# Optimization experiments

Measured on AMD Instinct MI355X. Metric: run time of the kernel, lower is better.

The kernel has to match this reference:

```python
import jax, jax.numpy as jnp
import numpy as np

N = 50000      # nodes
E = 400000     # edges (before self-loops)
DIN = 128
HID = 128
HEADS = 4
DOUT = 64
NEG_SLOPE = 0.2  # PyG GATConv default


def setup_inputs() -> dict:
    key = jax.random.key(0)
    ks = jax.random.split(key, 14)

    def w(k, shape, fan_in):
        return jax.random.normal(k, shape, dtype=jnp.float32) * (1.0 / np.sqrt(fan_in))

    x = jax.random.normal(ks[0], (N, DIN), dtype=jnp.float32)
    edge_index = jax.random.randint(ks[1], (2, E), 0, N, dtype=jnp.int32)

    # layer 1: DIN -> HEADS*HID (concat)
    W1 = w(ks[2], (DIN, HEADS * HID), DIN)
    a_src1 = w(ks[3], (HEADS, HID), HID)
    a_dst1 = w(ks[4], (HEADS, HID), HID)
    b1 = jnp.zeros((HEADS * HID,), jnp.float32)
    # layer 2: HEADS*HID -> HEADS*HID (concat)
    W2 = w(ks[5], (HEADS * HID, HEADS * HID), HEADS * HID)
    a_src2 = w(ks[6], (HEADS, HID), HID)
    a_dst2 = w(ks[7], (HEADS, HID), HID)
    b2 = jnp.zeros((HEADS * HID,), jnp.float32)
    # layer 3: HEADS*HID -> DOUT, heads=1, concat=False (mean)
    W3 = w(ks[8], (HEADS * HID, DOUT), HEADS * HID)
    a_src3 = w(ks[9], (1, DOUT), DOUT)
    a_dst3 = w(ks[10], (1, DOUT), DOUT)
    b3 = jnp.zeros((DOUT,), jnp.float32)

    return dict(x=x, edge_index=edge_index,
                W1=W1, a_src1=a_src1, a_dst1=a_dst1, b1=b1,
                W2=W2, a_src2=a_src2, a_dst2=a_dst2, b2=b2,
                W3=W3, a_src3=a_src3, a_dst3=a_dst3, b3=b3)


def _gat_layer(x, src, dst, W, a_src, a_dst, n):
    """One GATConv (eval mode, self-loops already in src/dst). Returns [n, H, C]."""
    H, C = a_src.shape
    h = (x @ W).reshape(n, H, C)                        # projected features
    alpha_s = jnp.einsum('nhc,hc->nh', h, a_src)        # per-node src logits
    alpha_d = jnp.einsum('nhc,hc->nh', h, a_dst)
    e = jax.nn.leaky_relu(alpha_s[src] + alpha_d[dst], NEG_SLOPE)  # [E', H]
    # segment softmax over incoming edges of each dst node
    m = jax.ops.segment_max(e, dst, num_segments=n)
    e = jnp.exp(e - m[dst])
    s = jax.ops.segment_sum(e, dst, num_segments=n)
    alpha = e / (s[dst] + 1e-16)                        # [E', H]
    msg = h[src] * alpha[:, :, None]                    # [E', H, C]
    return jax.ops.segment_sum(msg, dst, num_segments=n)


def reference(x, edge_index, W1, a_src1, a_dst1, b1,
              W2, a_src2, a_dst2, b2, W3, a_src3, a_dst3, b3):
    n = x.shape[0]
    loops = jnp.arange(n, dtype=edge_index.dtype)       # PyG add_self_loops=True
    src = jnp.concatenate([edge_index[0], loops])
    dst = jnp.concatenate([edge_index[1], loops])

    h = _gat_layer(x, src, dst, W1, a_src1, a_dst1, n).reshape(n, -1) + b1
    h = jax.nn.elu(h)   # dropout is identity in eval mode
    h = _gat_layer(h, src, dst, W2, a_src2, a_dst2, n).reshape(n, -1) + b2
    h = jax.nn.elu(h)
    out = _gat_layer(h, src, dst, W3, a_src3, a_dst3, n)[:, 0, :] + b3  # heads=1, concat=False
    return out
```

## Files before the change

kernel.cpp:

```cpp
#include <hip/hip_runtime.h>
#include <hip/hip_bf16.h>


typedef __attribute__((ext_vector_type(8))) short bf16x8;
typedef __attribute__((ext_vector_type(4))) float f32x4;

__device__ __forceinline__ float bflo(unsigned w) { return __uint_as_float(w << 16); }
__device__ __forceinline__ float bfhi(unsigned w) { return __uint_as_float(w & 0xffff0000u); }
__device__ __forceinline__ float leaky(float x) { return x > 0.f ? x : 0.2f * x; }
__device__ __forceinline__ unsigned pack2(float a, float b) {
    unsigned ua = __bfloat16_as_ushort(__float2bfloat16(a));
    unsigned ub = __bfloat16_as_ushort(__float2bfloat16(b));
    return ua | (ub << 16);
}


__global__ void k_count(const int* __restrict__ ei, int E, int N, int* __restrict__ cnt) {
    int e = blockIdx.x * blockDim.x + threadIdx.x;
    int tot = E + N;
    if (e >= tot) return;
    int d = (e < E) ? ei[E + e] : (e - E);
    atomicAdd(&cnt[d], 1);
}

__global__ void k_scan1(const int* __restrict__ cnt, int N, int* __restrict__ rp,
                        int* __restrict__ blksum) {
    __shared__ int sdata[256];
    int t = threadIdx.x;
    int base = blockIdx.x * 1024;
    int v[4];
    int loc = 0;
#pragma unroll
    for (int i = 0; i < 4; i++) {
        int idx = base + t * 4 + i;
        v[i] = (idx < N) ? ((cnt[idx] + 3) & ~3) : 0;
        loc += v[i];
    }
    int x = loc;
    sdata[t] = x;
    __syncthreads();
    for (int off = 1; off < 256; off <<= 1) {
        int y = (t >= off) ? sdata[t - off] : 0;
        __syncthreads();
        x += y;
        sdata[t] = x;
        __syncthreads();
    }
    int run = x - loc;
#pragma unroll
    for (int i = 0; i < 4; i++) {
        int idx = base + t * 4 + i;
        if (idx < N) rp[idx] = run;
        run += v[i];
    }
    if (t == 255) blksum[blockIdx.x] = x;
}

__global__ void k_scan2(const int* __restrict__ blksum, int nblk, int* __restrict__ blkoff) {
    int l = threadIdx.x;
    int v = (l < nblk) ? blksum[l] : 0;
    int x = v;
#pragma unroll
    for (int off = 1; off < 64; off <<= 1) {
        int y = __shfl_up(x, off);
        if (l >= off) x += y;
    }
    if (l < nblk) blkoff[l] = x - v;
}

__global__ void k_scan3(int* __restrict__ rp, const int* __restrict__ blkoff,
                        const int* __restrict__ blksum, const int* __restrict__ cnt,
                        int N, int nblk, int* __restrict__ cur,
                        int* __restrict__ col, int* __restrict__ dste) {
    int i = blockIdx.x * blockDim.x + threadIdx.x;
    if (i < N) {
        int v = rp[i] + blkoff[i >> 10];
        rp[i] = v;
        cur[i] = v;
        int c = cnt[i];
        int pad = ((c + 3) & ~3) - c;
        for (int p = 0; p < pad; p++) {
            col[v + c + p] = 0;
            dste[v + c + p] = -1;
        }
    }
    if (i == 0) rp[N] = blkoff[nblk - 1] + blksum[nblk - 1];
}

__global__ void k_fill(const int* __restrict__ ei, int E, int N, int* __restrict__ cur,
                       int* __restrict__ col, int* __restrict__ dste) {
    int e = blockIdx.x * blockDim.x + threadIdx.x;
    int tot = E + N;
    if (e >= tot) return;
    int s, d;
    if (e < E) { s = ei[e]; d = ei[E + e]; }
    else       { s = e - E; d = e - E; }
    int p = atomicAdd(&cur[d], 1);
    col[p] = s;
    dste[p] = d;
}


__global__ void k_cast_pad(const float* __restrict__ X, __hip_bfloat16* __restrict__ Xb,
                           int n_elems, int total) {
    int i = (blockIdx.x * blockDim.x + threadIdx.x) * 4;
    if (i >= total) return;
    float4 v = make_float4(0.f, 0.f, 0.f, 0.f);
    if (i < n_elems) v = *(const float4*)&X[i];
    __hip_bfloat16 tmp[4] = {__float2bfloat16(v.x), __float2bfloat16(v.y),
                             __float2bfloat16(v.z), __float2bfloat16(v.w)};
    *(ushort4*)&Xb[i] = *(const ushort4*)tmp;
}

__global__ void k_castT(const float* __restrict__ W, __hip_bfloat16* __restrict__ Wt,
                        int K, int Nw) {
    __shared__ float t[32][33];
    int k0 = blockIdx.x * 32, n0 = blockIdx.y * 32;
    int tx = threadIdx.x & 31, ty = threadIdx.x >> 5;
    for (int i = ty; i < 32; i += 8) t[i][tx] = W[(size_t)(k0 + i) * Nw + n0 + tx];
    __syncthreads();
    for (int i = ty; i < 32; i += 8)
        Wt[(size_t)(n0 + i) * K + k0 + tx] = __float2bfloat16(t[tx][i]);
}

__global__ void k_va1(const float* __restrict__ W1, const float* __restrict__ asrc,
                      const float* __restrict__ adst, float* __restrict__ va8) {
    int t = threadIdx.x;
    int c = t >> 2, h = t & 3;
    const float* wrow = W1 + (size_t)c * 512 + h * 128;
    const float* av = asrc + h * 128;
    const float* dv = adst + h * 128;
    float vs = 0.f, vd = 0.f;
    for (int k = 0; k < 128; k++) {
        float wv = wrow[k];
        vs += wv * av[k];
        vd += wv * dv[k];
    }
    va8[c * 8 + h] = vs;
    va8[c * 8 + 4 + h] = vd;
}

__global__ void k_alpha_x(const __hip_bfloat16* __restrict__ xb,
                          const float* __restrict__ va8, float* __restrict__ as_out,
                          float* __restrict__ ad_out, int N) {
    int w = (blockIdx.x * blockDim.x + threadIdx.x) >> 6;
    int lane = threadIdx.x & 63;
    if (w >= N) return;
    unsigned wrd = ((const unsigned*)xb)[(size_t)w * 64 + lane];
    float f0 = bflo(wrd), f1 = bfhi(wrd);
    int c0 = lane * 2;
    float4 vs0 = *(const float4*)&va8[c0 * 8];
    float4 vd0 = *(const float4*)&va8[c0 * 8 + 4];
    float4 vs1 = *(const float4*)&va8[(c0 + 1) * 8];
    float4 vd1 = *(const float4*)&va8[(c0 + 1) * 8 + 4];
    float s[8];
    s[0] = f0 * vs0.x + f1 * vs1.x;
    s[1] = f0 * vs0.y + f1 * vs1.y;
    s[2] = f0 * vs0.z + f1 * vs1.z;
    s[3] = f0 * vs0.w + f1 * vs1.w;
    s[4] = f0 * vd0.x + f1 * vd1.x;
    s[5] = f0 * vd0.y + f1 * vd1.y;
    s[6] = f0 * vd0.z + f1 * vd1.z;
    s[7] = f0 * vd0.w + f1 * vd1.w;
#pragma unroll
    for (int off = 32; off >= 1; off >>= 1)
#pragma unroll
        for (int j = 0; j < 8; j++) s[j] += __shfl_xor(s[j], off);
    if (lane == 0) {
        *(float4*)&as_out[w * 4] = make_float4(s[0], s[1], s[2], s[3]);
        *(float4*)&ad_out[w * 4] = make_float4(s[4], s[5], s[6], s[7]);
    }
}


template <int BN, bool FUSE>
__global__ void __launch_bounds__(256) k_gemm_mfma(const __hip_bfloat16* __restrict__ A,
                                                   const __hip_bfloat16* __restrict__ Bt,
                                                   __hip_bfloat16* __restrict__ C,
                                                   int lda, int ldc, int K,
                                                   int hsA, int hsB, int hsC,
                                                   const float* __restrict__ bias) {
    constexpr int BM = 128, BK = 64;
    constexpr int WM = 64;
    constexpr int WN = BN / 2;
    constexpr int MREP = WM / 16;
    constexpr int NREP = WN / 16;

    __shared__ __hip_bfloat16 lds[(BM + BN) * BK];
    __hip_bfloat16* As = lds;
    __hip_bfloat16* Bs = lds + BM * BK;

    const int z = blockIdx.z;
    A += (size_t)z * hsA;
    Bt += (size_t)z * hsB;
    const int cbase = z * hsC;

    const int tid = threadIdx.x;
    const int wave = tid >> 6;
    const int lane = tid & 63;
    const int wm0 = (wave >> 1) * WM;
    const int wn0 = (wave & 1) * WN;
    const int m0 = blockIdx.y * BM;
    const int n0 = blockIdx.x * BN;
    const int fr = lane & 15;
    const int fq = lane >> 4;

    f32x4 acc[MREP][NREP] = {};

    for (int kt = 0; kt < K; kt += BK) {
        const __hip_bfloat16* srcA = A + (size_t)m0 * lda + kt;
#pragma unroll
        for (int it = 0; it < BM * 8 / 256; ++it) {
            int gb = it * 256 + wave * 64;
            int g = gb + lane;
            int row = g >> 3;
            int kg = (g & 7) ^ (row & 7);
            const __hip_bfloat16* gsrc = srcA + (size_t)row * lda + kg * 8;
            __builtin_amdgcn_global_load_lds(
                (const __attribute__((address_space(1))) void*)gsrc,
                (__attribute__((address_space(3))) void*)(As + gb * 8), 16, 0, 0);
        }
        const __hip_bfloat16* srcB = Bt + (size_t)n0 * K + kt;
#pragma unroll
        for (int it = 0; it < BN * 8 / 256; ++it) {
            int gb = it * 256 + wave * 64;
            int g = gb + lane;
            int row = g >> 3;
            int kg = (g & 7) ^ (row & 7);
            const __hip_bfloat16* gsrc = srcB + (size_t)row * K + kg * 8;
            __builtin_amdgcn_global_load_lds(
                (const __attribute__((address_space(1))) void*)gsrc,
                (__attribute__((address_space(3))) void*)(Bs + gb * 8), 16, 0, 0);
        }
        __syncthreads();

#pragma unroll
        for (int sl = 0; sl < 2; ++sl) {
            int ke = sl * 32 + fq * 8;
            bf16x8 af[MREP], bfr[NREP];
#pragma unroll
            for (int i = 0; i < MREP; ++i) {
                int row = wm0 + i * 16 + fr;
                int e = (row * BK + ke) ^ ((row & 7) << 3);
                af[i] = *(const bf16x8*)(As + e);
            }
#pragma unroll
            for (int j = 0; j < NREP; ++j) {
                int row = wn0 + j * 16 + fr;
                int e = (row * BK + ke) ^ ((row & 7) << 3);
                bfr[j] = *(const bf16x8*)(Bs + e);
            }
#pragma unroll
            for (int i = 0; i < MREP; ++i)
#pragma unroll
                for (int j = 0; j < NREP; ++j)
                    acc[i][j] = __builtin_amdgcn_mfma_f32_16x16x32_bf16(
                        af[i], bfr[j], acc[i][j], 0, 0, 0);
        }
        __syncthreads();
    }

#pragma unroll
    for (int i = 0; i < MREP; ++i) {
#pragma unroll
        for (int j = 0; j < NREP; ++j) {
            int colg = cbase + n0 + wn0 + j * 16 + fr;
#pragma unroll
            for (int r = 0; r < 4; ++r) {
                int rowg = m0 + wm0 + i * 16 + fq * 4 + r;
                float v = acc[i][j][r];
                if (FUSE) {
                    v += bias[colg];
                    v = v > 0.f ? v : expm1f(v);
                }
                C[(size_t)rowg * ldc + colg] = __float2bfloat16(v);
            }
        }
    }
}


template <int C, int H>
__global__ void k_alpha(const __hip_bfloat16* __restrict__ h, const float* __restrict__ a_src,
                        const float* __restrict__ a_dst, float* __restrict__ as_out,
                        float* __restrict__ ad_out, int N) {
    int w = (blockIdx.x * blockDim.x + threadIdx.x) >> 6;
    int lane = threadIdx.x & 63;
    int n = w / H, hd = w % H;
    if (n >= N) return;
    const __hip_bfloat16* hp = h + (size_t)n * (C * H) + hd * C;
    const float* asp = a_src + hd * C;
    const float* adp = a_dst + hd * C;
    float s1 = 0.f, s2 = 0.f;
    if constexpr (C == 128) {
        unsigned wrd = *(const unsigned*)(hp + 2 * lane);
        float f0 = bflo(wrd), f1 = bfhi(wrd);
        float2 a2 = *(const float2*)(asp + 2 * lane);
        float2 d2 = *(const float2*)(adp + 2 * lane);
        s1 = f0 * a2.x + f1 * a2.y;
        s2 = f0 * d2.x + f1 * d2.y;
    } else {
        float v = __bfloat162float(hp[lane & 63]);
        s1 = v * asp[lane];
        s2 = v * adp[lane];
    }
#pragma unroll
    for (int off = 32; off >= 1; off >>= 1) {
        s1 += __shfl_xor(s1, off);
        s2 += __shfl_xor(s2, off);
    }
    if (lane == 0) {
        as_out[n * H + hd] = s1;
        ad_out[n * H + hd] = s2;
    }
}


__global__ void k_edgewA(const int* __restrict__ col, const int* __restrict__ dste,
                         const float* __restrict__ as, const float* __restrict__ ad,
                         float* __restrict__ wA, const int* __restrict__ rp, int N) {
    int e = blockIdx.x * blockDim.x + threadIdx.x;
    if (e >= rp[N]) return;
    int d = dste[e];
    if (d < 0) {
        *(float4*)&wA[e * 4] = make_float4(0.f, 0.f, 0.f, 0.f);
        return;
    }
    int s = col[e];
    float4 a = *(const float4*)&as[s * 4];
    float4 b = *(const float4*)&ad[d * 4];
    float4 w;
    w.x = __expf(leaky(a.x + b.x));
    w.y = __expf(leaky(a.y + b.y));
    w.z = __expf(leaky(a.z + b.z));
    w.w = __expf(leaky(a.w + b.w));
    *(float4*)&wA[e * 4] = w;
}


__global__ void k_edgewS(const int* __restrict__ col, const int* __restrict__ dste,
                         const float* __restrict__ as, const float* __restrict__ ad,
                         float* __restrict__ wS, const int* __restrict__ rp, int N, int EP) {
    int e = blockIdx.x * blockDim.x + threadIdx.x;
    if (e >= rp[N]) return;
    int d = dste[e];
    if (d < 0) {
        wS[e] = 0.f; wS[EP + e] = 0.f; wS[2 * EP + e] = 0.f; wS[3 * EP + e] = 0.f;
        return;
    }
    int s = col[e];
    float4 a = *(const float4*)&as[s * 4];
    float4 b = *(const float4*)&ad[d * 4];
    wS[e]          = __expf(leaky(a.x + b.x));
    wS[EP + e]     = __expf(leaky(a.y + b.y));
    wS[2 * EP + e] = __expf(leaky(a.z + b.z));
    wS[3 * EP + e] = __expf(leaky(a.w + b.w));
}

__global__ void k_edgew1(const int* __restrict__ col, const int* __restrict__ dste,
                         const float* __restrict__ as, const float* __restrict__ ad,
                         float* __restrict__ wS, const int* __restrict__ rp, int N) {
    int e = blockIdx.x * blockDim.x + threadIdx.x;
    if (e >= rp[N]) return;
    int d = dste[e];
    if (d < 0) { wS[e] = 0.f; return; }
    wS[e] = __expf(leaky(as[col[e]] + ad[d]));
}


__global__ void k_gatherX(const __hip_bfloat16* __restrict__ xb,
                          const float* __restrict__ wA, const int* __restrict__ rp,
                          const int* __restrict__ col, unsigned* __restrict__ out32, int N) {
    int w = (blockIdx.x * blockDim.x + threadIdx.x) >> 6;
    int lane = threadIdx.x & 63;
    if (w >= N) return;
    int d = w;
    int r0 = rp[d], r1 = rp[d + 1];
    const unsigned* xp = (const unsigned*)xb;

    float acc[8] = {};
    float ws0 = 0.f, ws1 = 0.f, ws2 = 0.f, ws3 = 0.f;
    for (int e = r0; e < r1; e += 4) {
        int4 c4 = *(const int4*)&col[e];
        float4 w0 = *(const float4*)&wA[e * 4];
        float4 w1 = *(const float4*)&wA[e * 4 + 4];
        float4 w2 = *(const float4*)&wA[e * 4 + 8];
        float4 w3 = *(const float4*)&wA[e * 4 + 12];
        unsigned v0 = xp[(size_t)c4.x * 64 + lane];
        unsigned v1 = xp[(size_t)c4.y * 64 + lane];
        unsigned v2 = xp[(size_t)c4.z * 64 + lane];
        unsigned v3 = xp[(size_t)c4.w * 64 + lane];
        ws0 += w0.x + w1.x + w2.x + w3.x;
        ws1 += w0.y + w1.y + w2.y + w3.y;
        ws2 += w0.z + w1.z + w2.z + w3.z;
        ws3 += w0.w + w1.w + w2.w + w3.w;
        float f0, f1;
        f0 = bflo(v0); f1 = bfhi(v0);
        acc[0] += w0.x * f0; acc[1] += w0.x * f1;
        acc[2] += w0.y * f0; acc[3] += w0.y * f1;
        acc[4] += w0.z * f0; acc[5] += w0.z * f1;
        acc[6] += w0.w * f0; acc[7] += w0.w * f1;
        f0 = bflo(v1); f1 = bfhi(v1);
        acc[0] += w1.x * f0; acc[1] += w1.x * f1;
        acc[2] += w1.y * f0; acc[3] += w1.y * f1;
        acc[4] += w1.z * f0; acc[5] += w1.z * f1;
        acc[6] += w1.w * f0; acc[7] += w1.w * f1;
        f0 = bflo(v2); f1 = bfhi(v2);
        acc[0] += w2.x * f0; acc[1] += w2.x * f1;
        acc[2] += w2.y * f0; acc[3] += w2.y * f1;
        acc[4] += w2.z * f0; acc[5] += w2.z * f1;
        acc[6] += w2.w * f0; acc[7] += w2.w * f1;
        f0 = bflo(v3); f1 = bfhi(v3);
        acc[0] += w3.x * f0; acc[1] += w3.x * f1;
        acc[2] += w3.y * f0; acc[3] += w3.y * f1;
        acc[4] += w3.z * f0; acc[5] += w3.z * f1;
        acc[6] += w3.w * f0; acc[7] += w3.w * f1;
    }
    float i0 = 1.f / (ws0 + 1e-16f), i1 = 1.f / (ws1 + 1e-16f);
    float i2 = 1.f / (ws2 + 1e-16f), i3 = 1.f / (ws3 + 1e-16f);
    size_t ob = (size_t)d * 256 + lane;
    out32[ob]       = pack2(acc[0] * i0, acc[1] * i0);
    out32[ob + 64]  = pack2(acc[2] * i1, acc[3] * i1);
    out32[ob + 128] = pack2(acc[4] * i2, acc[5] * i2);
    out32[ob + 192] = pack2(acc[6] * i3, acc[7] * i3);
}


__global__ void k_gatherH(const __hip_bfloat16* __restrict__ hfeat,
                          const float* __restrict__ wS, const int* __restrict__ rp,
                          const int* __restrict__ col, const float* __restrict__ bias,
                          unsigned* __restrict__ out32, int N, int EP) {
    int w = (blockIdx.x * blockDim.x + threadIdx.x) >> 6;
    int lane = threadIdx.x & 63;
    if (w >= N) return;
    int hd = blockIdx.z;
    int d = w;
    int r0 = rp[d], r1 = rp[d + 1];
    const float* wp = wS + (size_t)hd * EP;
    const unsigned* hp = (const unsigned*)hfeat;
    const int coff = hd * 64 + lane;

    float a0 = 0.f, a1 = 0.f, wsum = 0.f;
    for (int e = r0; e < r1; e += 4) {
        int4 c4 = *(const int4*)&col[e];
        float4 w4 = *(const float4*)&wp[e];
        unsigned v0 = hp[(size_t)c4.x * 256 + coff];
        unsigned v1 = hp[(size_t)c4.y * 256 + coff];
        unsigned v2 = hp[(size_t)c4.z * 256 + coff];
        unsigned v3 = hp[(size_t)c4.w * 256 + coff];
        wsum += (w4.x + w4.y) + (w4.z + w4.w);
        a0 += w4.x * bflo(v0); a1 += w4.x * bfhi(v0);
        a0 += w4.y * bflo(v1); a1 += w4.y * bfhi(v1);
        a0 += w4.z * bflo(v2); a1 += w4.z * bfhi(v2);
        a0 += w4.w * bflo(v3); a1 += w4.w * bfhi(v3);
    }
    float inv = 1.f / (wsum + 1e-16f);
    int c = hd * 128 + lane * 2;
    float o0 = a0 * inv + bias[c];
    float o1 = a1 * inv + bias[c + 1];
    o0 = o0 > 0.f ? o0 : expm1f(o0);
    o1 = o1 > 0.f ? o1 : expm1f(o1);
    out32[(size_t)d * 256 + coff] = pack2(o0, o1);
}


__global__ void k_gather64(const __hip_bfloat16* __restrict__ hfeat,
                           const float* __restrict__ wbuf, const int* __restrict__ rp,
                           const int* __restrict__ col, const float* __restrict__ bias,
                           float* __restrict__ out, int N) {
    int w = (blockIdx.x * blockDim.x + threadIdx.x) >> 6;
    int lane = threadIdx.x & 63;
    if (w >= N) return;
    int d = w;
    int r0 = rp[d], r1 = rp[d + 1];
    int g = lane >> 4, cl = lane & 15;

    float a0 = 0.f, a1 = 0.f, a2 = 0.f, a3 = 0.f, wsum = 0.f;
    for (int e0 = r0; e0 < r1; e0 += 4) {
        int e = e0 + g;
        int s = col[e];
        float wf = wbuf[e];
        uint2 q = *(const uint2*)(hfeat + (size_t)s * 64 + cl * 4);
        wsum += wf;
        a0 += wf * bflo(q.x);
        a1 += wf * bfhi(q.x);
        a2 += wf * bflo(q.y);
        a3 += wf * bfhi(q.y);
    }
#pragma unroll
    for (int off = 16; off <= 32; off <<= 1) {
        a0 += __shfl_xor(a0, off);
        a1 += __shfl_xor(a1, off);
        a2 += __shfl_xor(a2, off);
        a3 += __shfl_xor(a3, off);
        wsum += __shfl_xor(wsum, off);
    }
    if (g == 0) {
        float inv = 1.0f / (wsum + 1e-16f);
        float4 b4 = *(const float4*)&bias[cl * 4];
        float4 o = make_float4(a0 * inv + b4.x, a1 * inv + b4.y,
                               a2 * inv + b4.z, a3 * inv + b4.w);
        *(float4*)(out + (size_t)d * 64 + cl * 4) = o;
    }
}


extern "C" void kernel_launch(void* const* d_in, const int* in_sizes, int n_in,
                              void* d_out, int out_size, void* d_ws, size_t ws_size,
                              hipStream_t stream) {
    const float* x   = (const float*)d_in[0];
    const int*   ei  = (const int*)d_in[1];
    const float* W1  = (const float*)d_in[2];
    const float* as1 = (const float*)d_in[3];
    const float* ad1 = (const float*)d_in[4];
    const float* b1  = (const float*)d_in[5];
    const float* W2  = (const float*)d_in[6];
    const float* as2 = (const float*)d_in[7];
    const float* ad2 = (const float*)d_in[8];
    const float* b2  = (const float*)d_in[9];
    const float* W3  = (const float*)d_in[10];
    const float* as3 = (const float*)d_in[11];
    const float* ad3 = (const float*)d_in[12];
    const float* b3  = (const float*)d_in[13];

    const int N = in_sizes[0] / 128;
    const int E = in_sizes[1] / 2;
    const int Etot = E + N;
    const int EP = (Etot + 3 * N + 255) & ~255;
    const int Mp = (N + 127) & ~127;

    char* ws = (char*)d_ws;
    size_t off = 0;
    auto alloc = [&](size_t bytes) -> void* {
        void* p = ws + off;
        off = (off + bytes + 255) & ~(size_t)255;
        return p;
    };
    __hip_bfloat16* hbuf = (__hip_bfloat16*)alloc((size_t)Mp * 512 * 2);
    __hip_bfloat16* fbuf = (__hip_bfloat16*)alloc((size_t)Mp * 512 * 2);
    __hip_bfloat16* xagg = (__hip_bfloat16*)alloc((size_t)Mp * 512 * 2);
    __hip_bfloat16* xb   = (__hip_bfloat16*)alloc((size_t)Mp * 128 * 2);
    __hip_bfloat16* Wt1  = (__hip_bfloat16*)alloc((size_t)512 * 128 * 2);
    __hip_bfloat16* Wt2  = (__hip_bfloat16*)alloc((size_t)512 * 512 * 2);
    __hip_bfloat16* Wt3  = (__hip_bfloat16*)alloc((size_t)64 * 512 * 2);
    float* aS   = (float*)alloc((size_t)N * 4 * 4);
    float* aD   = (float*)alloc((size_t)N * 4 * 4);
    float* wbuf = (float*)alloc((size_t)EP * 4 * 4);
    float* va8  = (float*)alloc(128 * 8 * 4);
    int* cnt  = (int*)alloc((size_t)N * 4);
    int* rp   = (int*)alloc((size_t)(N + 1) * 4);
    int* cur  = (int*)alloc((size_t)N * 4);
    int* col  = (int*)alloc((size_t)EP * 4);
    int* dste = (int*)alloc((size_t)EP * 4);
    int* blks = (int*)alloc(64 * 4);
    int* blko = (int*)alloc(64 * 4);

    hipMemsetAsync(cnt, 0, (size_t)N * 4, stream);
    int thr = 256;
    k_count<<<(Etot + thr - 1) / thr, thr, 0, stream>>>(ei, E, N, cnt);
    int nblk = (N + 1023) / 1024;
    k_scan1<<<nblk, 256, 0, stream>>>(cnt, N, rp, blks);
    k_scan2<<<1, 64, 0, stream>>>(blks, nblk, blko);
    k_scan3<<<(N + 255) / 256, 256, 0, stream>>>(rp, blko, blks, cnt, N, nblk, cur, col, dste);
    k_fill<<<(Etot + thr - 1) / thr, thr, 0, stream>>>(ei, E, N, cur, col, dste);

    {
        int total = Mp * 128;
        k_cast_pad<<<(total / 4 + 255) / 256, 256, 0, stream>>>(x, xb, N * 128, total);
        dim3 g1(128 / 32, 512 / 32);
        k_castT<<<g1, 256, 0, stream>>>(W1, Wt1, 128, 512);
        dim3 g2(512 / 32, 512 / 32);
        k_castT<<<g2, 256, 0, stream>>>(W2, Wt2, 512, 512);
        dim3 g3(512 / 32, 64 / 32);
        k_castT<<<g3, 256, 0, stream>>>(W3, Wt3, 512, 64);
        k_va1<<<1, 512, 0, stream>>>(W1, as1, ad1, va8);
    }

    int alphaBlocks4 = (int)(((size_t)N * 4 * 64 + 255) / 256);
    int alphaBlocks1 = (int)(((size_t)N * 64 + 255) / 256);
    int edgeBlocks = (EP + 255) / 256;
    int gatBlocks = (N + 3) / 4;

    k_alpha_x<<<gatBlocks, 256, 0, stream>>>(xb, va8, aS, aD, N);
    k_edgewA<<<edgeBlocks, 256, 0, stream>>>(col, dste, aS, aD, wbuf, rp, N);
    k_gatherX<<<gatBlocks, 256, 0, stream>>>(xb, wbuf, rp, col, (unsigned*)xagg, N);
    {
        dim3 g(1, Mp / 128, 4);
        k_gemm_mfma<128, true><<<g, 256, 0, stream>>>(xagg, Wt1, fbuf,
                                                      512, 512, 128,
                                                      128, 128 * 128, 128, b1);
    }

    {
        dim3 g(4, Mp / 128, 1);
        k_gemm_mfma<128, false><<<g, 256, 0, stream>>>(fbuf, Wt2, hbuf,
                                                       512, 512, 512, 0, 0, 0, nullptr);
    }
    k_alpha<128, 4><<<alphaBlocks4, 256, 0, stream>>>(hbuf, as2, ad2, aS, aD, N);
    k_edgewS<<<edgeBlocks, 256, 0, stream>>>(col, dste, aS, aD, wbuf, rp, N, EP);
    {
        dim3 g(gatBlocks, 1, 4);
        k_gatherH<<<g, 256, 0, stream>>>(hbuf, wbuf, rp, col, b2, (unsigned*)fbuf, N, EP);
    }

    {
        dim3 g(1, Mp / 128, 1);
        k_gemm_mfma<64, false><<<g, 256, 0, stream>>>(fbuf, Wt3, hbuf,
                                                      512, 64, 512, 0, 0, 0, nullptr);
    }
    k_alpha<64, 1><<<alphaBlocks1, 256, 0, stream>>>(hbuf, as3, ad3, aS, aD, N);
    k_edgew1<<<edgeBlocks, 256, 0, stream>>>(col, dste, aS, aD, wbuf, rp, N);
    k_gather64<<<gatBlocks, 256, 0, stream>>>(hbuf, wbuf, rp, col, b3, (float*)d_out, N);
}
```

Baseline: 417.8 us.

## Merge per-head gather launches into one 512-wide gather with software prefetch

```diff
diff --git a/kernel.cpp b/kernel.cpp
--- a/kernel.cpp
+++ b/kernel.cpp
@@ -426,41 +426,72 @@
 }
 
 
-__global__ void k_gatherH(const __hip_bfloat16* __restrict__ hfeat,
-                          const float* __restrict__ wS, const int* __restrict__ rp,
-                          const int* __restrict__ col, const float* __restrict__ bias,
-                          unsigned* __restrict__ out32, int N, int EP) {
+template <bool DO_ELU>
+__global__ void k_gather512(const __hip_bfloat16* __restrict__ hfeat,
+                            const float* __restrict__ wS, const int* __restrict__ rp,
+                            const int* __restrict__ col, const float* __restrict__ bias,
+                            __hip_bfloat16* __restrict__ out, int N, int EP) {
     int w = (blockIdx.x * blockDim.x + threadIdx.x) >> 6;
     int lane = threadIdx.x & 63;
     if (w >= N) return;
-    int hd = blockIdx.z;
     int d = w;
     int r0 = rp[d], r1 = rp[d + 1];
-    const float* wp = wS + (size_t)hd * EP;
-    const unsigned* hp = (const unsigned*)hfeat;
-    const int coff = hd * 64 + lane;
-
-    float a0 = 0.f, a1 = 0.f, wsum = 0.f;
+    const float* wp = wS + (size_t)(lane >> 4) * EP;
+    const uint4* hp = (const uint4*)hfeat;
+
+    float acc[8] = {};
+    float wsum = 0.f;
+
+    int4 cA = *(const int4*)&col[r0];
+    float4 wq = *(const float4*)&wp[r0];
+    uint4 vA0 = hp[(size_t)cA.x * 64 + lane];
+    uint4 vA1 = hp[(size_t)cA.y * 64 + lane];
+    uint4 vA2 = hp[(size_t)cA.z * 64 + lane];
+    uint4 vA3 = hp[(size_t)cA.w * 64 + lane];
+    int eB = (r0 + 4 < r1) ? r0 + 4 : r0;
+    int4 cB = *(const int4*)&col[eB];
+    float4 wqB = *(const float4*)&wp[eB];
+
     for (int e = r0; e < r1; e += 4) {
-        int4 c4 = *(const int4*)&col[e];
-        float4 w4 = *(const float4*)&wp[e];
-        unsigned v0 = hp[(size_t)c4.x * 256 + coff];
-        unsigned v1 = hp[(size_t)c4.y * 256 + coff];
-        unsigned v2 = hp[(size_t)c4.z * 256 + coff];
-        unsigned v3 = hp[(size_t)c4.w * 256 + coff];
-        wsum += (w4.x + w4.y) + (w4.z + w4.w);
-        a0 += w4.x * bflo(v0); a1 += w4.x * bfhi(v0);
-        a0 += w4.y * bflo(v1); a1 += w4.y * bfhi(v1);
-        a0 += w4.z * bflo(v2); a1 += w4.z * bfhi(v2);
-        a0 += w4.w * bflo(v3); a1 += w4.w * bfhi(v3);
-    }
-    float inv = 1.f / (wsum + 1e-16f);
-    int c = hd * 128 + lane * 2;
-    float o0 = a0 * inv + bias[c];
-    float o1 = a1 * inv + bias[c + 1];
-    o0 = o0 > 0.f ? o0 : expm1f(o0);
-    o1 = o1 > 0.f ? o1 : expm1f(o1);
-    out32[(size_t)d * 256 + coff] = pack2(o0, o1);
+        int eC = (e + 8 < r1) ? e + 8 : r0;
+        uint4 nb0 = hp[(size_t)cB.x * 64 + lane];
+        uint4 nb1 = hp[(size_t)cB.y * 64 + lane];
+        uint4 nb2 = hp[(size_t)cB.z * 64 + lane];
+        uint4 nb3 = hp[(size_t)cB.w * 64 + lane];
+        int4 cC = *(const int4*)&col[eC];
+        float4 wqC = *(const float4*)&wp[eC];
+
+        wsum += (wq.x + wq.y) + (wq.z + wq.w);
+        acc[0] += wq.x * bflo(vA0.x); acc[1] += wq.x * bfhi(vA0.x);
+        acc[2] += wq.x * bflo(vA0.y); acc[3] += wq.x * bfhi(vA0.y);
+        acc[4] += wq.x * bflo(vA0.z); acc[5] += wq.x * bfhi(vA0.z);
+        acc[6] += wq.x * bflo(vA0.w); acc[7] += wq.x * bfhi(vA0.w);
+        acc[0] += wq.y * bflo(vA1.x); acc[1] += wq.y * bfhi(vA1.x);
+        acc[2] += wq.y * bflo(vA1.y); acc[3] += wq.y * bfhi(vA1.y);
+        acc[4] += wq.y * bflo(vA1.z); acc[5] += wq.y * bfhi(vA1.z);
+        acc[6] += wq.y * bflo(vA1.w); acc[7] += wq.y * bfhi(vA1.w);
+        acc[0] += wq.z * bflo(vA2.x); acc[1] += wq.z * bfhi(vA2.x);
+        acc[2] += wq.z * bflo(vA2.y); acc[3] += wq.z * bfhi(vA2.y);
+        acc[4] += wq.z * bflo(vA2.z); acc[5] += wq.z * bfhi(vA2.z);
+        acc[6] += wq.z * bflo(vA2.w); acc[7] += wq.z * bfhi(vA2.w);
+        acc[0] += wq.w * bflo(vA3.x); acc[1] += wq.w * bfhi(vA3.x);
+        acc[2] += wq.w * bflo(vA3.y); acc[3] += wq.w * bfhi(vA3.y);
+        acc[4] += wq.w * bflo(vA3.z); acc[5] += wq.w * bfhi(vA3.z);
+        acc[6] += wq.w * bflo(vA3.w); acc[7] += wq.w * bfhi(vA3.w);
+
+        wq = wqB; wqB = wqC; cB = cC;
+        vA0 = nb0; vA1 = nb1; vA2 = nb2; vA3 = nb3;
+    }
+
+    float inv = 1.0f / (wsum + 1e-16f);
+    __hip_bfloat16 tmp[8];
+#pragma unroll
+    for (int j = 0; j < 8; j++) {
+        float v = acc[j] * inv + bias[lane * 8 + j];
+        if (DO_ELU) v = v > 0.f ? v : expm1f(v);
+        tmp[j] = __float2bfloat16(v);
+    }
+    *(float4*)(out + (size_t)d * 512 + lane * 8) = *(const float4*)tmp;
 }
 
 
@@ -526,7 +557,7 @@
     const int N = in_sizes[0] / 128;
     const int E = in_sizes[1] / 2;
     const int Etot = E + N;
-    const int EP = (Etot + 3 * N + 255) & ~255;
+    const int EP = (Etot + 3 * N + 1024 + 255) & ~255;
     const int Mp = (N + 127) & ~127;
 
     char* ws = (char*)d_ws;
@@ -598,10 +629,7 @@
     }
     k_alpha<128, 4><<<alphaBlocks4, 256, 0, stream>>>(hbuf, as2, ad2, aS, aD, N);
     k_edgewS<<<edgeBlocks, 256, 0, stream>>>(col, dste, aS, aD, wbuf, rp, N, EP);
-    {
-        dim3 g(gatBlocks, 1, 4);
-        k_gatherH<<<g, 256, 0, stream>>>(hbuf, wbuf, rp, col, b2, (unsigned*)fbuf, N, EP);
-    }
+    k_gather512<true><<<gatBlocks, 256, 0, stream>>>(hbuf, wbuf, rp, col, b2, fbuf, N, EP);
 
     {
         dim3 g(1, Mp / 128, 1);
```

After: 416.7 us. About the same (-0.3%).

## Fuse edge-weight computation into gathers and widen layer-2 gather to all heads

Applied to the files above, without the earlier changes.

```diff
diff --git a/kernel.cpp b/kernel.cpp
--- a/kernel.cpp
+++ b/kernel.cpp
@@ -173,15 +173,15 @@
 }
 
 
-template <int BN, bool FUSE>
+template <int BM, int BN, bool FUSE>
 __global__ void __launch_bounds__(256) k_gemm_mfma(const __hip_bfloat16* __restrict__ A,
                                                    const __hip_bfloat16* __restrict__ Bt,
                                                    __hip_bfloat16* __restrict__ C,
                                                    int lda, int ldc, int K,
                                                    int hsA, int hsB, int hsC,
                                                    const float* __restrict__ bias) {
-    constexpr int BM = 128, BK = 64;
-    constexpr int WM = 64;
+    constexpr int BK = 64;
+    constexpr int WM = BM / 2;
     constexpr int WN = BN / 2;
     constexpr int MREP = WM / 16;
     constexpr int NREP = WN / 16;
@@ -335,36 +335,6 @@
     w.z = __expf(leaky(a.z + b.z));
     w.w = __expf(leaky(a.w + b.w));
     *(float4*)&wA[e * 4] = w;
-}
-
-
-__global__ void k_edgewS(const int* __restrict__ col, const int* __restrict__ dste,
-                         const float* __restrict__ as, const float* __restrict__ ad,
-                         float* __restrict__ wS, const int* __restrict__ rp, int N, int EP) {
-    int e = blockIdx.x * blockDim.x + threadIdx.x;
-    if (e >= rp[N]) return;
-    int d = dste[e];
-    if (d < 0) {
-        wS[e] = 0.f; wS[EP + e] = 0.f; wS[2 * EP + e] = 0.f; wS[3 * EP + e] = 0.f;
-        return;
-    }
-    int s = col[e];
-    float4 a = *(const float4*)&as[s * 4];
-    float4 b = *(const float4*)&ad[d * 4];
-    wS[e]          = __expf(leaky(a.x + b.x));
-    wS[EP + e]     = __expf(leaky(a.y + b.y));
-    wS[2 * EP + e] = __expf(leaky(a.z + b.z));
-    wS[3 * EP + e] = __expf(leaky(a.w + b.w));
-}
-
-__global__ void k_edgew1(const int* __restrict__ col, const int* __restrict__ dste,
-                         const float* __restrict__ as, const float* __restrict__ ad,
-                         float* __restrict__ wS, const int* __restrict__ rp, int N) {
-    int e = blockIdx.x * blockDim.x + threadIdx.x;
-    if (e >= rp[N]) return;
-    int d = dste[e];
-    if (d < 0) { wS[e] = 0.f; return; }
-    wS[e] = __expf(leaky(as[col[e]] + ad[d]));
 }
 
 
@@ -426,46 +396,72 @@
 }
 
 
-__global__ void k_gatherH(const __hip_bfloat16* __restrict__ hfeat,
-                          const float* __restrict__ wS, const int* __restrict__ rp,
-                          const int* __restrict__ col, const float* __restrict__ bias,
-                          unsigned* __restrict__ out32, int N, int EP) {
+template <bool DO_ELU>
+__global__ void k_gather512(const __hip_bfloat16* __restrict__ hfeat,
+                            const float* __restrict__ as4, const float* __restrict__ ad4,
+                            const int* __restrict__ cnt, const int* __restrict__ rp,
+                            const int* __restrict__ col, const float* __restrict__ bias,
+                            __hip_bfloat16* __restrict__ out, int N) {
     int w = (blockIdx.x * blockDim.x + threadIdx.x) >> 6;
     int lane = threadIdx.x & 63;
     if (w >= N) return;
-    int hd = blockIdx.z;
     int d = w;
     int r0 = rp[d], r1 = rp[d + 1];
-    const float* wp = wS + (size_t)hd * EP;
-    const unsigned* hp = (const unsigned*)hfeat;
-    const int coff = hd * 64 + lane;
-
-    float a0 = 0.f, a1 = 0.f, wsum = 0.f;
+    int r1r = r0 + cnt[d];
+    int hd = lane >> 4;
+    float adv = ad4[d * 4 + hd];
+    const uint4* hp = (const uint4*)hfeat;
+
+    float acc[8] = {};
+    float wsum = 0.f;
     for (int e = r0; e < r1; e += 4) {
         int4 c4 = *(const int4*)&col[e];
-        float4 w4 = *(const float4*)&wp[e];
-        unsigned v0 = hp[(size_t)c4.x * 256 + coff];
-        unsigned v1 = hp[(size_t)c4.y * 256 + coff];
-        unsigned v2 = hp[(size_t)c4.z * 256 + coff];
-        unsigned v3 = hp[(size_t)c4.w * 256 + coff];
-        wsum += (w4.x + w4.y) + (w4.z + w4.w);
-        a0 += w4.x * bflo(v0); a1 += w4.x * bfhi(v0);
-        a0 += w4.y * bflo(v1); a1 += w4.y * bfhi(v1);
-        a0 += w4.z * bflo(v2); a1 += w4.z * bfhi(v2);
-        a0 += w4.w * bflo(v3); a1 += w4.w * bfhi(v3);
-    }
-    float inv = 1.f / (wsum + 1e-16f);
-    int c = hd * 128 + lane * 2;
-    float o0 = a0 * inv + bias[c];
-    float o1 = a1 * inv + bias[c + 1];
-    o0 = o0 > 0.f ? o0 : expm1f(o0);
-    o1 = o1 > 0.f ? o1 : expm1f(o1);
-    out32[(size_t)d * 256 + coff] = pack2(o0, o1);
+        float l0 = as4[c4.x * 4 + hd] + adv;
+        float l1 = as4[c4.y * 4 + hd] + adv;
+        float l2 = as4[c4.z * 4 + hd] + adv;
+        float l3 = as4[c4.w * 4 + hd] + adv;
+        uint4 v0 = hp[(size_t)c4.x * 64 + lane];
+        uint4 v1 = hp[(size_t)c4.y * 64 + lane];
+        uint4 v2 = hp[(size_t)c4.z * 64 + lane];
+        uint4 v3 = hp[(size_t)c4.w * 64 + lane];
+        float w0 = (e + 0 < r1r) ? __expf(leaky(l0)) : 0.f;
+        float w1 = (e + 1 < r1r) ? __expf(leaky(l1)) : 0.f;
+        float w2 = (e + 2 < r1r) ? __expf(leaky(l2)) : 0.f;
+        float w3 = (e + 3 < r1r) ? __expf(leaky(l3)) : 0.f;
+        wsum += (w0 + w1) + (w2 + w3);
+        acc[0] += w0 * bflo(v0.x); acc[1] += w0 * bfhi(v0.x);
+        acc[2] += w0 * bflo(v0.y); acc[3] += w0 * bfhi(v0.y);
+        acc[4] += w0 * bflo(v0.z); acc[5] += w0 * bfhi(v0.z);
+        acc[6] += w0 * bflo(v0.w); acc[7] += w0 * bfhi(v0.w);
+        acc[0] += w1 * bflo(v1.x); acc[1] += w1 * bfhi(v1.x);
+        acc[2] += w1 * bflo(v1.y); acc[3] += w1 * bfhi(v1.y);
+        acc[4] += w1 * bflo(v1.z); acc[5] += w1 * bfhi(v1.z);
+        acc[6] += w1 * bflo(v1.w); acc[7] += w1 * bfhi(v1.w);
+        acc[0] += w2 * bflo(v2.x); acc[1] += w2 * bfhi(v2.x);
+        acc[2] += w2 * bflo(v2.y); acc[3] += w2 * bfhi(v2.y);
+        acc[4] += w2 * bflo(v2.z); acc[5] += w2 * bfhi(v2.z);
+        acc[6] += w2 * bflo(v2.w); acc[7] += w2 * bfhi(v2.w);
+        acc[0] += w3 * bflo(v3.x); acc[1] += w3 * bfhi(v3.x);
+        acc[2] += w3 * bflo(v3.y); acc[3] += w3 * bfhi(v3.y);
+        acc[4] += w3 * bflo(v3.z); acc[5] += w3 * bfhi(v3.z);
+        acc[6] += w3 * bflo(v3.w); acc[7] += w3 * bfhi(v3.w);
+    }
+
+    float inv = 1.0f / (wsum + 1e-16f);
+    __hip_bfloat16 tmp[8];
+#pragma unroll
+    for (int j = 0; j < 8; j++) {
+        float v = acc[j] * inv + bias[lane * 8 + j];
+        if (DO_ELU) v = v > 0.f ? v : expm1f(v);
+        tmp[j] = __float2bfloat16(v);
+    }
+    *(float4*)(out + (size_t)d * 512 + lane * 8) = *(const float4*)tmp;
 }
 
 
 __global__ void k_gather64(const __hip_bfloat16* __restrict__ hfeat,
-                           const float* __restrict__ wbuf, const int* __restrict__ rp,
+                           const float* __restrict__ as1, const float* __restrict__ ad1,
+                           const int* __restrict__ cnt, const int* __restrict__ rp,
                            const int* __restrict__ col, const float* __restrict__ bias,
                            float* __restrict__ out, int N) {
     int w = (blockIdx.x * blockDim.x + threadIdx.x) >> 6;
@@ -473,14 +469,17 @@
     if (w >= N) return;
     int d = w;
     int r0 = rp[d], r1 = rp[d + 1];
+    int r1r = r0 + cnt[d];
+    float adv = ad1[d];
     int g = lane >> 4, cl = lane & 15;
 
     float a0 = 0.f, a1 = 0.f, a2 = 0.f, a3 = 0.f, wsum = 0.f;
     for (int e0 = r0; e0 < r1; e0 += 4) {
         int e = e0 + g;
         int s = col[e];
-        float wf = wbuf[e];
+        float l = as1[s] + adv;
         uint2 q = *(const uint2*)(hfeat + (size_t)s * 64 + cl * 4);
+        float wf = (e < r1r) ? __expf(leaky(l)) : 0.f;
         wsum += wf;
         a0 += wf * bflo(q.x);
         a1 += wf * bfhi(q.x);
@@ -586,29 +585,25 @@
     k_gatherX<<<gatBlocks, 256, 0, stream>>>(xb, wbuf, rp, col, (unsigned*)xagg, N);
     {
         dim3 g(1, Mp / 128, 4);
-        k_gemm_mfma<128, true><<<g, 256, 0, stream>>>(xagg, Wt1, fbuf,
-                                                      512, 512, 128,
-                                                      128, 128 * 128, 128, b1);
+        k_gemm_mfma<128, 128, true><<<g, 256, 0, stream>>>(xagg, Wt1, fbuf,
+                                                           512, 512, 128,
+                                                           128, 128 * 128, 128, b1);
     }
 
     {
         dim3 g(4, Mp / 128, 1);
-        k_gemm_mfma<128, false><<<g, 256, 0, stream>>>(fbuf, Wt2, hbuf,
-                                                       512, 512, 512, 0, 0, 0, nullptr);
+        k_gemm_mfma<128, 128, false><<<g, 256, 0, stream>>>(fbuf, Wt2, hbuf,
+                                                            512, 512, 512, 0, 0, 0, nullptr);
     }
     k_alpha<128, 4><<<alphaBlocks4, 256, 0, stream>>>(hbuf, as2, ad2, aS, aD, N);
-    k_edgewS<<<edgeBlocks, 256, 0, stream>>>(col, dste, aS, aD, wbuf, rp, N, EP);
+    k_gather512<true><<<gatBlocks, 256, 0, stream>>>(hbuf, aS, aD, cnt, rp, col, b2, fbuf, N);
+
     {
-        dim3 g(gatBlocks, 1, 4);
-        k_gatherH<<<g, 256, 0, stream>>>(hbuf, wbuf, rp, col, b2, (unsigned*)fbuf, N, EP);
-    }
-
-    {
-        dim3 g(1, Mp / 128, 1);
-        k_gemm_mfma<64, false><<<g, 256, 0, stream>>>(fbuf, Wt3, hbuf,
-                                                      512, 64, 512, 0, 0, 0, nullptr);
+        dim3 g(1, Mp / 64, 1);
+        k_gemm_mfma<64, 64, false><<<g, 256, 0, stream>>>(fbuf, Wt3, hbuf,
+                                                          512, 64, 512, 0, 0, 0, nullptr);
     }
     k_alpha<64, 1><<<alphaBlocks1, 256, 0, stream>>>(hbuf, as3, ad3, aS, aD, N);
-    k_edgew1<<<edgeBlocks, 256, 0, stream>>>(col, dste, aS, aD, wbuf, rp, N);
-    k_gather64<<<gatBlocks, 256, 0, stream>>>(hbuf, wbuf, rp, col, b3, (float*)d_out, N);
-}
+    k_gather64<<<gatBlocks, 256, 0, stream>>>(hbuf, aS, aD, cnt, rp, col, b3,
+                                              (float*)d_out, N);
+}
```

Result: faster. 408.2 us (-2.3%).
